# Optimization experiments

Hardware: AMD Instinct MI355X
Metric: run time of the kernel (lower is better)

Reference implementation:

```python
import jax, jax.numpy as jnp
import numpy as np

NUM_HEADS = 16
HIDDEN = 1024
HEAD_DIM = HIDDEN // NUM_HEADS


def setup_inputs() -> dict:
    key = jax.random.key(0)
    ks = jax.random.split(key, 9)
    B, S = 2, 2048
    scale = 1.0 / np.sqrt(HIDDEN)
    x = jax.random.normal(ks[0], (B, S, HIDDEN), dtype=jnp.float32)
    Wq = jax.random.uniform(ks[1], (HIDDEN, HIDDEN), jnp.float32, -scale, scale)
    bq = jax.random.uniform(ks[2], (HIDDEN,), jnp.float32, -scale, scale)
    Wk = jax.random.uniform(ks[3], (HIDDEN, HIDDEN), jnp.float32, -scale, scale)
    bk = jax.random.uniform(ks[4], (HIDDEN,), jnp.float32, -scale, scale)
    Wv = jax.random.uniform(ks[5], (HIDDEN, HIDDEN), jnp.float32, -scale, scale)
    bv = jax.random.uniform(ks[6], (HIDDEN,), jnp.float32, -scale, scale)
    Wo = jax.random.uniform(ks[7], (HIDDEN, HIDDEN), jnp.float32, -scale, scale)
    bo = jax.random.uniform(ks[8], (HIDDEN,), jnp.float32, -scale, scale)
    return {"x": x, "Wq": Wq, "bq": bq, "Wk": Wk, "bk": bk,
            "Wv": Wv, "bv": bv, "Wo": Wo, "bo": bo}


def reference(x, Wq, bq, Wk, bk, Wv, bv, Wo, bo):
    B, S, _ = x.shape
    H, D = NUM_HEADS, HEAD_DIM
    # projections (torch Linear: x @ W^T + b)
    q = (x @ Wq.T + bq).reshape(B, S, H, D).transpose(0, 2, 1, 3)  # [B,H,S,D]
    k = (x @ Wk.T + bk).reshape(B, S, H, D).transpose(0, 2, 1, 3)
    v = (x @ Wv.T + bv).reshape(B, S, H, D).transpose(0, 2, 1, 3)
    scores = jnp.einsum("bhqd,bhkd->bhqk", q, k) / jnp.sqrt(jnp.float32(D))
    causal = jnp.tril(jnp.ones((S, S), dtype=bool))  # True = keep
    scores = jnp.where(causal, scores, -jnp.inf)
    weights = jax.nn.softmax(scores, axis=-1)
    out = jnp.einsum("bhqk,bhkd->bhqd", weights, v)  # [B,H,S,D]
    out = out.transpose(0, 2, 1, 3).reshape(B, S, H * D)
    return out @ Wo.T + bo
```

## Files before the change

kernel.cpp:

```cpp
#include <hip/hip_runtime.h>
#include <stdint.h>


#define HIDDEN 1024
#define NH 16
#define HD 64
#define BATCH 2
#define SEQ 2048

typedef unsigned short u16;
typedef unsigned int u32;
typedef __attribute__((ext_vector_type(8))) short short8;
typedef __attribute__((ext_vector_type(4))) float f32x4;

typedef const __attribute__((address_space(1))) u32 gu32;
typedef __attribute__((address_space(3))) u32 lu32;

__device__ __forceinline__ u16 f2bf(float f) {
    u32 u = __float_as_uint(f);
    return (u16)((u + 0x7FFFu + ((u >> 16) & 1u)) >> 16);
}

__global__ void cvt_all(const float* __restrict__ x, const float* __restrict__ Wq,
                        const float* __restrict__ Wk, const float* __restrict__ Wv,
                        const float* __restrict__ Wo, u16* __restrict__ xb,
                        u16* __restrict__ wqb, u16* __restrict__ wkb,
                        u16* __restrict__ wvb, u16* __restrict__ wob) {
    const int blk = blockIdx.x;
    const float* src; u16* dst; int base;
    if (blk < 2048)      { src = x;  dst = xb;  base = blk; }
    else if (blk < 2560) { src = Wq; dst = wqb; base = blk - 2048; }
    else if (blk < 3072) { src = Wk; dst = wkb; base = blk - 2560; }
    else if (blk < 3584) { src = Wv; dst = wvb; base = blk - 3072; }
    else                 { src = Wo; dst = wob; base = blk - 3584; }
    const int i = base * 256 + threadIdx.x;
    float4 a = ((const float4*)src)[2 * i];
    float4 b = ((const float4*)src)[2 * i + 1];
    union { u16 h[8]; uint4 v; } o;
    o.h[0] = f2bf(a.x); o.h[1] = f2bf(a.y); o.h[2] = f2bf(a.z); o.h[3] = f2bf(a.w);
    o.h[4] = f2bf(b.x); o.h[5] = f2bf(b.y); o.h[6] = f2bf(b.z); o.h[7] = f2bf(b.w);
    ((uint4*)dst)[i] = o.v;
}

__device__ __forceinline__ void stage16(const u16* __restrict__ G, int grow0,
                                        int k0, u16* lds, int rbase, int lane) {
    const int sr = lane >> 2;
    const int lc = (lane & 3) ^ (sr & 3);
    const u16* g = G + (size_t)(grow0 + rbase + sr) * 1024 + k0 + lc * 8;
    __builtin_amdgcn_global_load_lds((gu32*)g, (lu32*)(lds + rbase * 32), 16, 0, 0);
}

__launch_bounds__(256, 3)
__global__ void gemm_qkv(const u16* __restrict__ A, const u16* __restrict__ Wqb,
                         const u16* __restrict__ Wkb, const u16* __restrict__ Wvb,
                         const float* __restrict__ bq, const float* __restrict__ bk,
                         const float* __restrict__ bv, u16* __restrict__ Qo,
                         u16* __restrict__ Ko, u16* __restrict__ Vo) {
    __shared__ u16 As[2][128 * 32];
    __shared__ u16 Bs[2][128 * 32];
    const int which = blockIdx.x >> 3;
    const int n0 = (blockIdx.x & 7) * 128;
    const int m0 = blockIdx.y * 128;
    const u16* Wt = (which == 0) ? Wqb : (which == 1) ? Wkb : Wvb;
    const float* bias = (which == 0) ? bq : (which == 1) ? bk : bv;
    u16* out = (which == 0) ? Qo : (which == 1) ? Ko : Vo;
    const float oscale = (which == 0) ? 0.18033688011112042f : 1.0f;
    const int t = threadIdx.x;
    const int lane = t & 63, w = t >> 6, quad = lane >> 4, lm = lane & 15;
    const int wm = (w & 1) * 64, wn = (w >> 1) * 64;

    f32x4 acc[4][4] = {};

    auto stage = [&](int k0, int buf) {
        stage16(A, m0, k0, As[buf], w * 32, lane);
        stage16(A, m0, k0, As[buf], w * 32 + 16, lane);
        stage16(Wt, n0, k0, Bs[buf], w * 32, lane);
        stage16(Wt, n0, k0, Bs[buf], w * 32 + 16, lane);
    };

    stage(0, 0);
    __syncthreads();
    for (int k0 = 0; k0 < 1024; k0 += 32) {
        const int cur = (k0 >> 5) & 1;
        if (k0 + 32 < 1024) stage(k0 + 32, cur ^ 1);
        short8 af[4], bf[4];
        const int sw = (quad ^ (lm & 3)) * 8;
#pragma unroll
        for (int mi = 0; mi < 4; mi++)
            af[mi] = *(const short8*)(&As[cur][(wm + mi * 16 + lm) * 32] + sw);
#pragma unroll
        for (int ni = 0; ni < 4; ni++)
            bf[ni] = *(const short8*)(&Bs[cur][(wn + ni * 16 + lm) * 32] + sw);
#pragma unroll
        for (int mi = 0; mi < 4; mi++)
#pragma unroll
            for (int ni = 0; ni < 4; ni++)
                acc[mi][ni] = __builtin_amdgcn_mfma_f32_16x16x32_bf16(
                    af[mi], bf[ni], acc[mi][ni], 0, 0, 0);
        __syncthreads();
    }

#pragma unroll
    for (int ni = 0; ni < 4; ni++) {
        const int n = n0 + wn + ni * 16 + lm;
        const float bv_ = bias[n];
        const int h = n >> 6, d = n & 63;
#pragma unroll
        for (int mi = 0; mi < 4; mi++)
#pragma unroll
            for (int r = 0; r < 4; r++) {
                const int m = m0 + wm + mi * 16 + quad * 4 + r;
                const int b = m >> 11, s = m & 2047;
                const u16 hv = f2bf((acc[mi][ni][r] + bv_) * oscale);
                if (which == 2)
                    out[(((size_t)(b * NH + h) * HD + d) * SEQ) + s] = hv;
                else
                    out[(((size_t)(b * NH + h) * SEQ + s) * HD) + d] = hv;
            }
    }
}

__launch_bounds__(256, 2)
__global__ void gemm_out(const u16* __restrict__ A, const u16* __restrict__ Wt,
                         const float* __restrict__ bias, float* __restrict__ out) {
    __shared__ u16 As[2][64 * 32];
    __shared__ u16 Bs[2][128 * 32];
    const int n0 = blockIdx.x * 128;
    const int m0 = blockIdx.y * 64;
    const int t = threadIdx.x;
    const int lane = t & 63, w = t >> 6, quad = lane >> 4, lm = lane & 15;
    const int wm = (w & 1) * 32, wn = (w >> 1) * 64;

    f32x4 acc[2][4] = {};

    auto stage = [&](int k0, int buf) {
        stage16(A, m0, k0, As[buf], w * 16, lane);
        stage16(Wt, n0, k0, Bs[buf], w * 32, lane);
        stage16(Wt, n0, k0, Bs[buf], w * 32 + 16, lane);
    };

    stage(0, 0);
    __syncthreads();
    for (int k0 = 0; k0 < 1024; k0 += 32) {
        const int cur = (k0 >> 5) & 1;
        if (k0 + 32 < 1024) stage(k0 + 32, cur ^ 1);
        short8 af[2], bf[4];
        const int sw = (quad ^ (lm & 3)) * 8;
#pragma unroll
        for (int mi = 0; mi < 2; mi++)
            af[mi] = *(const short8*)(&As[cur][(wm + mi * 16 + lm) * 32] + sw);
#pragma unroll
        for (int ni = 0; ni < 4; ni++)
            bf[ni] = *(const short8*)(&Bs[cur][(wn + ni * 16 + lm) * 32] + sw);
#pragma unroll
        for (int mi = 0; mi < 2; mi++)
#pragma unroll
            for (int ni = 0; ni < 4; ni++)
                acc[mi][ni] = __builtin_amdgcn_mfma_f32_16x16x32_bf16(
                    af[mi], bf[ni], acc[mi][ni], 0, 0, 0);
        __syncthreads();
    }

#pragma unroll
    for (int ni = 0; ni < 4; ni++) {
        const int n = n0 + wn + ni * 16 + lm;
        const float bv_ = bias[n];
#pragma unroll
        for (int mi = 0; mi < 2; mi++)
#pragma unroll
            for (int r = 0; r < 4; r++) {
                const int m = m0 + wm + mi * 16 + quad * 4 + r;
                out[(size_t)m * 1024 + n] = acc[mi][ni][r] + bv_;
            }
    }
}

__launch_bounds__(256, 3)
__global__ void attn_kernel(const u16* __restrict__ Q, const u16* __restrict__ K,
                            const u16* __restrict__ Vt, u16* __restrict__ Out) {
    constexpr int LDP = 68;
    __shared__ u16 Ks[2][64 * 64];
    __shared__ u16 Vs[2][64 * 64];
    __shared__ u16 Ps[4 * 16 * LDP];
    const int t = threadIdx.x;
    const int lane = t & 63, w = t >> 6, quad = lane >> 4, lm = lane & 15;
    const int qt = 31 - (blockIdx.x >> 5);
    const int bh = blockIdx.x & 31;
    const int b = bh >> 4, h = bh & 15;
    const size_t base = (size_t)(b * NH + h) * SEQ * HD;
    const u16* Qg = Q + base;
    const u16* Kg = K + base;
    const u16* Vg = Vt + base;
    const int q0 = qt * 64 + w * 16;
    const int nk = qt + 1;

    short8 qf[2];
#pragma unroll
    for (int kk = 0; kk < 2; kk++)
        qf[kk] = *(const short8*)(Qg + (size_t)(q0 + lm) * HD + kk * 32 + quad * 8);

    f32x4 oacc[4] = {};
    f32x4 lacc = {};
    short8 ones;
#pragma unroll
    for (int j = 0; j < 8; j++) ones[j] = (short)0x3F80;

    u16* Pw = Ps + w * 16 * LDP;

    const int srow = (lane >> 3);
    const int schunk = (lane & 7) ^ srow;
    auto stage_kv = [&](int kt, int buf) {
#pragma unroll
        for (int j = 0; j < 2; j++) {
            const int row = w * 16 + j * 8 + srow;
            const u16* gk = Kg + (size_t)(kt * 64 + row) * HD + schunk * 8;
            const u16* gv = Vg + (size_t)row * SEQ + kt * 64 + schunk * 8;
            __builtin_amdgcn_global_load_lds((gu32*)gk, (lu32*)(&Ks[buf][(w * 16 + j * 8) * 64]), 16, 0, 0);
            __builtin_amdgcn_global_load_lds((gu32*)gv, (lu32*)(&Vs[buf][(w * 16 + j * 8) * 64]), 16, 0, 0);
        }
    };

    auto compute_step = [&](const u16* Kc, const u16* Vc, int kt_) {
        f32x4 sacc[4];
#pragma unroll
        for (int n = 0; n < 4; n++) {
            const int r = n * 16 + lm;
            const u16* rowp = Kc + r * 64;
            short8 kf0 = *(const short8*)(rowp + ((quad ^ (r & 7)) * 8));
            short8 kf1 = *(const short8*)(rowp + (((quad + 4) ^ (r & 7)) * 8));
            f32x4 a = {};
            a = __builtin_amdgcn_mfma_f32_16x16x32_bf16(qf[0], kf0, a, 0, 0, 0);
            a = __builtin_amdgcn_mfma_f32_16x16x32_bf16(qf[1], kf1, a, 0, 0, 0);
            sacc[n] = a;
        }
        if (kt_ == qt) {
#pragma unroll
            for (int n = 0; n < 4; n++)
#pragma unroll
                for (int r = 0; r < 4; r++)
                    if (n * 16 + lm > w * 16 + quad * 4 + r)
                        sacc[n][r] = -__builtin_inff();
        }
#pragma unroll
        for (int n = 0; n < 4; n++)
#pragma unroll
            for (int r = 0; r < 4; r++)
                Pw[(quad * 4 + r) * LDP + n * 16 + lm] =
                    (u16)(__float_as_uint(exp2f(sacc[n][r])) >> 16);
        short8 pf[2];
#pragma unroll
        for (int k4 = 0; k4 < 2; k4++)
            pf[k4] = *(const short8*)(Pw + lm * LDP + k4 * 32 + quad * 8);
#pragma unroll
        for (int n = 0; n < 4; n++) {
            const int r = n * 16 + lm;
            const u16* rowp = Vc + r * 64;
#pragma unroll
            for (int k4 = 0; k4 < 2; k4++) {
                short8 vf = *(const short8*)(rowp + (((k4 * 4 + quad) ^ (r & 7)) * 8));
                oacc[n] = __builtin_amdgcn_mfma_f32_16x16x32_bf16(pf[k4], vf, oacc[n], 0, 0, 0);
            }
        }
#pragma unroll
        for (int k4 = 0; k4 < 2; k4++)
            lacc = __builtin_amdgcn_mfma_f32_16x16x32_bf16(pf[k4], ones, lacc, 0, 0, 0);
    };

    stage_kv(0, 0);
    __syncthreads();

    for (int kt = 0; kt < nk; kt++) {
        const int cur = kt & 1;
        if (kt + 1 < nk) stage_kv(kt + 1, cur ^ 1);
        compute_step(Ks[cur], Vs[cur], kt);
        __syncthreads();
    }

    float inv[4];
#pragma unroll
    for (int r = 0; r < 4; r++) inv[r] = 1.0f / lacc[r];
#pragma unroll
    for (int n = 0; n < 4; n++)
#pragma unroll
        for (int r = 0; r < 4; r++) {
            const int qq = q0 + quad * 4 + r;
            Out[(size_t)(b * SEQ + qq) * HIDDEN + h * HD + n * 16 + lm] =
                f2bf(oacc[n][r] * inv[r]);
        }
}

extern "C" void kernel_launch(void* const* d_in, const int* in_sizes, int n_in,
                              void* d_out, int out_size, void* d_ws, size_t ws_size,
                              hipStream_t stream) {
    const float* x  = (const float*)d_in[0];
    const float* Wq = (const float*)d_in[1];
    const float* bq = (const float*)d_in[2];
    const float* Wk = (const float*)d_in[3];
    const float* bk = (const float*)d_in[4];
    const float* Wv = (const float*)d_in[5];
    const float* bv = (const float*)d_in[6];
    const float* Wo = (const float*)d_in[7];
    const float* bo = (const float*)d_in[8];
    float* out = (float*)d_out;

    char* ws = (char*)d_ws;
    const size_t SZ_X = (size_t)4096 * 1024 * 2;
    const size_t SZ_W = (size_t)1024 * 1024 * 2;
    u16* xb    = (u16*)(ws);
    u16* wqb   = (u16*)(ws + SZ_X);
    u16* wkb   = (u16*)(ws + SZ_X + SZ_W);
    u16* wvb   = (u16*)(ws + SZ_X + 2 * SZ_W);
    u16* wob   = (u16*)(ws + SZ_X + 3 * SZ_W);
    u16* Qb    = (u16*)(ws + SZ_X + 4 * SZ_W);
    u16* Kb    = (u16*)(ws + 2 * SZ_X + 4 * SZ_W);
    u16* Vtb   = (u16*)(ws + 3 * SZ_X + 4 * SZ_W);
    u16* attnb = (u16*)(ws + 4 * SZ_X + 4 * SZ_W);

    cvt_all<<<4096, 256, 0, stream>>>(x, Wq, Wk, Wv, Wo, xb, wqb, wkb, wvb, wob);
    gemm_qkv<<<dim3(24, 32), 256, 0, stream>>>(xb, wqb, wkb, wvb, bq, bk, bv, Qb, Kb, Vtb);
    attn_kernel<<<BATCH * NH * (SEQ / 64), 256, 0, stream>>>(Qb, Kb, Vtb, attnb);
    gemm_out<<<dim3(8, 64), 256, 0, stream>>>(attnb, wob, bo, out);
}
```

Baseline: 200.6 us.

## Load K and V fragments directly from global memory instead of LDS staging

Drops the double-buffered LDS staging of K and V tiles and the per-iteration block barrier in the attention kernel. Each wave now reads its K and V MFMA fragments straight from global memory, relying on L1/L2 caching because all four waves read the same tile. Launch bounds are raised to four blocks per SM to use the freed LDS. The cost is redundant global and cache traffic (each wave fetches the full tile) and no prefetch overlap, so load latency is exposed unless occupancy hides it.

```diff
diff --git a/kernel.cpp b/kernel.cpp
--- a/kernel.cpp
+++ b/kernel.cpp
@@ -175,12 +175,10 @@
     }
 }
 
-__launch_bounds__(256, 3)
+__launch_bounds__(256, 4)
 __global__ void attn_kernel(const u16* __restrict__ Q, const u16* __restrict__ K,
                             const u16* __restrict__ Vt, u16* __restrict__ Out) {
     constexpr int LDP = 68;
-    __shared__ u16 Ks[2][64 * 64];
-    __shared__ u16 Vs[2][64 * 64];
     __shared__ u16 Ps[4 * 16 * LDP];
     const int t = threadIdx.x;
     const int lane = t & 63, w = t >> 6, quad = lane >> 4, lm = lane & 15;
@@ -207,33 +205,26 @@
 
     u16* Pw = Ps + w * 16 * LDP;
 
-    const int srow = (lane >> 3);
-    const int schunk = (lane & 7) ^ srow;
-    auto stage_kv = [&](int kt, int buf) {
-#pragma unroll
-        for (int j = 0; j < 2; j++) {
-            const int row = w * 16 + j * 8 + srow;
-            const u16* gk = Kg + (size_t)(kt * 64 + row) * HD + schunk * 8;
-            const u16* gv = Vg + (size_t)row * SEQ + kt * 64 + schunk * 8;
-            __builtin_amdgcn_global_load_lds((gu32*)gk, (lu32*)(&Ks[buf][(w * 16 + j * 8) * 64]), 16, 0, 0);
-            __builtin_amdgcn_global_load_lds((gu32*)gv, (lu32*)(&Vs[buf][(w * 16 + j * 8) * 64]), 16, 0, 0);
-        }
-    };
-
-    auto compute_step = [&](const u16* Kc, const u16* Vc, int kt_) {
+    for (int kt = 0; kt < nk; kt++) {
+        const u16* Kt = Kg + (size_t)(kt * 64) * HD;
+        const u16* Vtp = Vg + kt * 64;
+
+        short8 kf0[4], kf1[4];
+#pragma unroll
+        for (int n = 0; n < 4; n++) {
+            const u16* rowp = Kt + (size_t)(n * 16 + lm) * HD;
+            kf0[n] = *(const short8*)(rowp + quad * 8);
+            kf1[n] = *(const short8*)(rowp + 32 + quad * 8);
+        }
         f32x4 sacc[4];
 #pragma unroll
         for (int n = 0; n < 4; n++) {
-            const int r = n * 16 + lm;
-            const u16* rowp = Kc + r * 64;
-            short8 kf0 = *(const short8*)(rowp + ((quad ^ (r & 7)) * 8));
-            short8 kf1 = *(const short8*)(rowp + (((quad + 4) ^ (r & 7)) * 8));
             f32x4 a = {};
-            a = __builtin_amdgcn_mfma_f32_16x16x32_bf16(qf[0], kf0, a, 0, 0, 0);
-            a = __builtin_amdgcn_mfma_f32_16x16x32_bf16(qf[1], kf1, a, 0, 0, 0);
+            a = __builtin_amdgcn_mfma_f32_16x16x32_bf16(qf[0], kf0[n], a, 0, 0, 0);
+            a = __builtin_amdgcn_mfma_f32_16x16x32_bf16(qf[1], kf1[n], a, 0, 0, 0);
             sacc[n] = a;
         }
-        if (kt_ == qt) {
+        if (kt == qt) {
 #pragma unroll
             for (int n = 0; n < 4; n++)
 #pragma unroll
@@ -253,27 +244,16 @@
             pf[k4] = *(const short8*)(Pw + lm * LDP + k4 * 32 + quad * 8);
 #pragma unroll
         for (int n = 0; n < 4; n++) {
-            const int r = n * 16 + lm;
-            const u16* rowp = Vc + r * 64;
+            const u16* rowp = Vtp + (size_t)(n * 16 + lm) * SEQ;
 #pragma unroll
             for (int k4 = 0; k4 < 2; k4++) {
-                short8 vf = *(const short8*)(rowp + (((k4 * 4 + quad) ^ (r & 7)) * 8));
+                short8 vf = *(const short8*)(rowp + (k4 * 4 + quad) * 8);
                 oacc[n] = __builtin_amdgcn_mfma_f32_16x16x32_bf16(pf[k4], vf, oacc[n], 0, 0, 0);
             }
         }
 #pragma unroll
         for (int k4 = 0; k4 < 2; k4++)
             lacc = __builtin_amdgcn_mfma_f32_16x16x32_bf16(pf[k4], ones, lacc, 0, 0, 0);
-    };
-
-    stage_kv(0, 0);
-    __syncthreads();
-
-    for (int kt = 0; kt < nk; kt++) {
-        const int cur = kt & 1;
-        if (kt + 1 < nk) stage_kv(kt + 1, cur ^ 1);
-        compute_step(Ks[cur], Vs[cur], kt);
-        __syncthreads();
     }
 
     float inv[4];
```

Result: slower. 293.7 us (+46.4%).

## Double attention query tile to 128 rows per block with two m-subtiles per wave

Applied to the files above, without the earlier changes.

Each attention block now handles 128 query rows (32 per wave, as two 16-row subtiles) instead of 64, so each staged K/V tile feeds twice as many MFMAs and K/V traffic through LDS and global memory is halved. The grid shrinks to 512 blocks. Block-to-tile mapping is rewritten so the two grid halves walk query tiles in opposite order, to balance the causal workload. This raises register and LDS use per block, which may lower occupancy under the 3-blocks launch bound, and the diagonal masking now covers two key tiles.

```diff
diff --git a/kernel.cpp b/kernel.cpp
--- a/kernel.cpp
+++ b/kernel.cpp
@@ -181,31 +181,35 @@
     constexpr int LDP = 68;
     __shared__ u16 Ks[2][64 * 64];
     __shared__ u16 Vs[2][64 * 64];
-    __shared__ u16 Ps[4 * 16 * LDP];
+    __shared__ u16 Ps[4 * 32 * LDP];
     const int t = threadIdx.x;
     const int lane = t & 63, w = t >> 6, quad = lane >> 4, lm = lane & 15;
-    const int qt = 31 - (blockIdx.x >> 5);
-    const int bh = blockIdx.x & 31;
+    const int pair = blockIdx.x & 255;
+    const int half = blockIdx.x >> 8;
+    const int qt = half ? (pair & 15) : (15 - (pair & 15));
+    const int bh = (pair >> 4) | (half << 4);
     const int b = bh >> 4, h = bh & 15;
     const size_t base = (size_t)(b * NH + h) * SEQ * HD;
     const u16* Qg = Q + base;
     const u16* Kg = K + base;
     const u16* Vg = Vt + base;
-    const int q0 = qt * 64 + w * 16;
-    const int nk = qt + 1;
-
-    short8 qf[2];
-#pragma unroll
-    for (int kk = 0; kk < 2; kk++)
-        qf[kk] = *(const short8*)(Qg + (size_t)(q0 + lm) * HD + kk * 32 + quad * 8);
-
-    f32x4 oacc[4] = {};
-    f32x4 lacc = {};
+    const int q0 = qt * 128 + w * 32;
+    const int nk = 2 * qt + 2;
+
+    short8 qf[2][2];
+#pragma unroll
+    for (int m = 0; m < 2; m++)
+#pragma unroll
+        for (int kk = 0; kk < 2; kk++)
+            qf[m][kk] = *(const short8*)(Qg + (size_t)(q0 + m * 16 + lm) * HD + kk * 32 + quad * 8);
+
+    f32x4 oacc[2][4] = {};
+    f32x4 lacc[2] = {};
     short8 ones;
 #pragma unroll
     for (int j = 0; j < 8; j++) ones[j] = (short)0x3F80;
 
-    u16* Pw = Ps + w * 16 * LDP;
+    u16* Pw = Ps + w * 32 * LDP;
 
     const int srow = (lane >> 3);
     const int schunk = (lane & 7) ^ srow;
@@ -221,36 +225,46 @@
     };
 
     auto compute_step = [&](const u16* Kc, const u16* Vc, int kt_) {
-        f32x4 sacc[4];
+        f32x4 sacc[2][4];
 #pragma unroll
         for (int n = 0; n < 4; n++) {
             const int r = n * 16 + lm;
             const u16* rowp = Kc + r * 64;
             short8 kf0 = *(const short8*)(rowp + ((quad ^ (r & 7)) * 8));
             short8 kf1 = *(const short8*)(rowp + (((quad + 4) ^ (r & 7)) * 8));
-            f32x4 a = {};
-            a = __builtin_amdgcn_mfma_f32_16x16x32_bf16(qf[0], kf0, a, 0, 0, 0);
-            a = __builtin_amdgcn_mfma_f32_16x16x32_bf16(qf[1], kf1, a, 0, 0, 0);
-            sacc[n] = a;
+#pragma unroll
+            for (int m = 0; m < 2; m++) {
+                f32x4 a = {};
+                a = __builtin_amdgcn_mfma_f32_16x16x32_bf16(qf[m][0], kf0, a, 0, 0, 0);
+                a = __builtin_amdgcn_mfma_f32_16x16x32_bf16(qf[m][1], kf1, a, 0, 0, 0);
+                sacc[m][n] = a;
+            }
         }
-        if (kt_ == qt) {
+        if (kt_ >= 2 * qt) {
+            const int kb = kt_ * 64 - qt * 128 - w * 32;
+#pragma unroll
+            for (int m = 0; m < 2; m++)
+#pragma unroll
+                for (int n = 0; n < 4; n++)
+#pragma unroll
+                    for (int r = 0; r < 4; r++)
+                        if (kb + n * 16 + lm > m * 16 + quad * 4 + r)
+                            sacc[m][n][r] = -__builtin_inff();
+        }
+#pragma unroll
+        for (int m = 0; m < 2; m++)
 #pragma unroll
             for (int n = 0; n < 4; n++)
 #pragma unroll
                 for (int r = 0; r < 4; r++)
-                    if (n * 16 + lm > w * 16 + quad * 4 + r)
-                        sacc[n][r] = -__builtin_inff();
-        }
-#pragma unroll
-        for (int n = 0; n < 4; n++)
-#pragma unroll
-            for (int r = 0; r < 4; r++)
-                Pw[(quad * 4 + r) * LDP + n * 16 + lm] =
-                    (u16)(__float_as_uint(exp2f(sacc[n][r])) >> 16);
-        short8 pf[2];
-#pragma unroll
-        for (int k4 = 0; k4 < 2; k4++)
-            pf[k4] = *(const short8*)(Pw + lm * LDP + k4 * 32 + quad * 8);
+                    Pw[(m * 16 + quad * 4 + r) * LDP + n * 16 + lm] =
+                        (u16)(__float_as_uint(exp2f(sacc[m][n][r])) >> 16);
+        short8 pf[2][2];
+#pragma unroll
+        for (int m = 0; m < 2; m++)
+#pragma unroll
+            for (int k4 = 0; k4 < 2; k4++)
+                pf[m][k4] = *(const short8*)(Pw + (m * 16 + lm) * LDP + k4 * 32 + quad * 8);
 #pragma unroll
         for (int n = 0; n < 4; n++) {
             const int r = n * 16 + lm;
@@ -258,12 +272,16 @@
 #pragma unroll
             for (int k4 = 0; k4 < 2; k4++) {
                 short8 vf = *(const short8*)(rowp + (((k4 * 4 + quad) ^ (r & 7)) * 8));
-                oacc[n] = __builtin_amdgcn_mfma_f32_16x16x32_bf16(pf[k4], vf, oacc[n], 0, 0, 0);
+#pragma unroll
+                for (int m = 0; m < 2; m++)
+                    oacc[m][n] = __builtin_amdgcn_mfma_f32_16x16x32_bf16(pf[m][k4], vf, oacc[m][n], 0, 0, 0);
             }
         }
 #pragma unroll
-        for (int k4 = 0; k4 < 2; k4++)
-            lacc = __builtin_amdgcn_mfma_f32_16x16x32_bf16(pf[k4], ones, lacc, 0, 0, 0);
+        for (int m = 0; m < 2; m++)
+#pragma unroll
+            for (int k4 = 0; k4 < 2; k4++)
+                lacc[m] = __builtin_amdgcn_mfma_f32_16x16x32_bf16(pf[m][k4], ones, lacc[m], 0, 0, 0);
     };
 
     stage_kv(0, 0);
@@ -276,17 +294,20 @@
         __syncthreads();
     }
 
-    float inv[4];
-#pragma unroll
-    for (int r = 0; r < 4; r++) inv[r] = 1.0f / lacc[r];
-#pragma unroll
-    for (int n = 0; n < 4; n++)
-#pragma unroll
-        for (int r = 0; r < 4; r++) {
-            const int qq = q0 + quad * 4 + r;
-            Out[(size_t)(b * SEQ + qq) * HIDDEN + h * HD + n * 16 + lm] =
-                f2bf(oacc[n][r] * inv[r]);
-        }
+#pragma unroll
+    for (int m = 0; m < 2; m++) {
+        float inv[4];
+#pragma unroll
+        for (int r = 0; r < 4; r++) inv[r] = 1.0f / lacc[m][r];
+#pragma unroll
+        for (int n = 0; n < 4; n++)
+#pragma unroll
+            for (int r = 0; r < 4; r++) {
+                const int qq = q0 + m * 16 + quad * 4 + r;
+                Out[(size_t)(b * SEQ + qq) * HIDDEN + h * HD + n * 16 + lm] =
+                    f2bf(oacc[m][n][r] * inv[r]);
+            }
+    }
 }
 
 extern "C" void kernel_launch(void* const* d_in, const int* in_sizes, int n_in,
@@ -318,6 +339,6 @@
 
     cvt_all<<<4096, 256, 0, stream>>>(x, Wq, Wk, Wv, Wo, xb, wqb, wkb, wvb, wob);
     gemm_qkv<<<dim3(24, 32), 256, 0, stream>>>(xb, wqb, wkb, wvb, bq, bk, bv, Qb, Kb, Vtb);
-    attn_kernel<<<BATCH * NH * (SEQ / 64), 256, 0, stream>>>(Qb, Kb, Vtb, attnb);
+    attn_kernel<<<BATCH * NH * (SEQ / 128), 256, 0, stream>>>(Qb, Kb, Vtb, attnb);
     gemm_out<<<dim3(8, 64), 256, 0, stream>>>(attnb, wob, bo, out);
 }
```

Result: slower. 217.7 us (+8.5%).
